# Kernel optimization log

Measured on AMD Instinct MI355X. Metric: run time of the kernel, lower is better.

## Reference

```python
import jax, jax.numpy as jnp
import numpy as np
import math

B, F, NB, H1, H2, K = 16384, 64, 64, 128, 128, 3
LN_EPS = 1e-5


def setup_inputs() -> dict:
    key = jax.random.key(0)
    ks = jax.random.split(key, 16)
    x = jax.random.normal(ks[0], (B, F), dtype=jnp.float32)
    # RBF params (per feature): centers init linspace(-3,3), log_widths = log(step)
    centers = jnp.broadcast_to(jnp.linspace(-3.0, 3.0, NB), (F, NB)).astype(jnp.float32)
    step = 6.0 / (NB - 1)
    log_widths = jnp.full((F, NB), math.log(step), dtype=jnp.float32)
    def lin(k, shape, fan_in):
        return jax.random.normal(k, shape, dtype=jnp.float32) / np.sqrt(fan_in)
    W1 = lin(ks[1], (F, NB, H1), NB); b1 = jnp.zeros((F, H1), jnp.float32)
    g1 = jnp.ones((F, H1), jnp.float32); be1 = jnp.zeros((F, H1), jnp.float32)
    W2 = lin(ks[2], (F, H1, H2), H1); b2 = jnp.zeros((F, H2), jnp.float32)
    g2 = jnp.ones((F, H2), jnp.float32); be2 = jnp.zeros((F, H2), jnp.float32)
    Wr = lin(ks[3], (F, NB, H2), NB); br = jnp.zeros((F, H2), jnp.float32)
    att = jnp.zeros((F,), jnp.float32)
    bias = jnp.zeros((H2,), jnp.float32)
    Wpi = lin(ks[4], (H2, K), H2); bpi = jnp.zeros((K,), jnp.float32)
    Wa = lin(ks[5], (H2, K), H2); ba = jnp.zeros((K,), jnp.float32)
    Wb = lin(ks[6], (H2, K), H2); bb = jnp.zeros((K,), jnp.float32)
    return dict(x=x, centers=centers, log_widths=log_widths, W1=W1, b1=b1, g1=g1,
                be1=be1, W2=W2, b2=b2, g2=g2, be2=be2, Wr=Wr, br=br, att=att,
                bias=bias, Wpi=Wpi, bpi=bpi, Wa=Wa, ba=ba, Wb=Wb, bb=bb)


def _layernorm(h, g, b):
    mu = jnp.mean(h, axis=-1, keepdims=True)
    var = jnp.mean((h - mu) ** 2, axis=-1, keepdims=True)
    return (h - mu) * jax.lax.rsqrt(var + LN_EPS) * g + b


def reference(x, centers, log_widths, W1, b1, g1, be1, W2, b2, g2, be2, Wr, br,
              att, bias, Wpi, bpi, Wa, ba, Wb, bb):
    # RBF expansion, feature axis batched: x [B,F] -> [B,F,NB]
    xc = jnp.clip(x, -10.0, 10.0)
    widths = jnp.exp(jnp.clip(log_widths, -5.0, 5.0)) + 0.1  # [F,NB]
    dist = (xc[:, :, None] - centers[None]) / widths[None]
    rbf = jnp.exp(-0.5 * jnp.clip(dist, -10.0, 10.0) ** 2)  # [B,F,NB]
    # per-feature MLP (grouped GEMMs via einsum)
    h = jnp.einsum('bfn,fnh->bfh', rbf, W1) + b1[None]
    h = jax.nn.gelu(_layernorm(h, g1[None], be1[None]), approximate=False)
    h = jnp.einsum('bfh,fhk->bfk', h, W2) + b2[None]
    h = jax.nn.gelu(_layernorm(h, g2[None], be2[None]), approximate=False)
    res = jnp.einsum('bfn,fnh->bfh', rbf, Wr) + br[None]
    stacked = h + 0.1 * res  # [B,F,H2]
    # attention-weighted aggregation over features
    w = jax.nn.softmax(att)
    agg = jnp.einsum('bfh,f->bh', stacked, w) + bias  # [B,H2]
    # mixture-beta head
    pi = jax.nn.softmax(agg @ Wpi + bpi, axis=-1)
    alpha = jnp.clip(jax.nn.softplus(agg @ Wa + ba) + 1.01, 1.01, 100.0)
    beta = jnp.clip(jax.nn.softplus(agg @ Wb + bb) + 1.01, 1.01, 100.0)
    pred = jnp.sum(pi * (alpha / (alpha + beta)), axis=-1)
    return jnp.clip(pred, 0.001, 0.999)
```

## Files before the change

### kernel.cpp

```cpp
#include <hip/hip_runtime.h>
#include <math.h>

#define BQ   16384
#define FQ   64
#define NBQ  64
#define HD   128
#define FG   4
#define FPG  16
#define MT   128
#define NT   512

typedef __attribute__((ext_vector_type(8))) short s16x8;
typedef __attribute__((ext_vector_type(4))) float f32x4;

__device__ __forceinline__ unsigned short f2bf(float x) {
    unsigned int u = __float_as_uint(x);
    return (unsigned short)((u + 0x7FFFu + ((u >> 16) & 1u)) >> 16);
}

__device__ __forceinline__ unsigned cvtpk_bf16(float lo, float hi) {
    unsigned r;
    asm("v_cvt_pk_bf16_f32 %0, %1, %2" : "=v"(r) : "v"(lo), "v"(hi));
    return r;
}

__device__ __forceinline__ float softplus_stable(float v) {
    return (v > 0.0f) ? (v + log1pf(expf(-v))) : log1pf(expf(v));
}

__device__ __forceinline__ f32x4 gelu4(f32x4 v) {
    const f32x4 v2 = v * v;
    const f32x4 tt = v2 * (-0.07135481f) + (-1.5957691f);
    const f32x4 s  = v * tt;
    f32x4 r;
    r[0] = __fdividef(v[0], 1.0f + __expf(s[0]));
    r[1] = __fdividef(v[1], 1.0f + __expf(s[1]));
    r[2] = __fdividef(v[2], 1.0f + __expf(s[2]));
    r[3] = __fdividef(v[3], 1.0f + __expf(s[3]));
    return r;
}

__device__ __forceinline__ void load16_lds(const unsigned short* g, unsigned short* l) {
    __builtin_amdgcn_global_load_lds(
        (const __attribute__((address_space(1))) unsigned int*)(uintptr_t)g,
        (__attribute__((address_space(3))) unsigned int*)(uintptr_t)l,
        16, 0, 0);
}


__global__ void __launch_bounds__(256) prep_misc(
    const float* __restrict__ att, const float* __restrict__ log_widths,
    const float* __restrict__ centers, const float* __restrict__ br,
    const float* __restrict__ bias,
    const float* __restrict__ b1, const float* __restrict__ g1, const float* __restrict__ be1,
    const float* __restrict__ b2, const float* __restrict__ g2, const float* __restrict__ be2,
    float* __restrict__ wsoft, float* __restrict__ crw2, float* __restrict__ rbias,
    float* __restrict__ Pk)
{
    const int t = threadIdx.x;
    if (blockIdx.x == 0) {
        __shared__ float ws[64];
        if (t < 64) {
            float v = att[t];
            float m = v;
#pragma unroll
            for (int s = 32; s >= 1; s >>= 1) m = fmaxf(m, __shfl_xor(m, s, 64));
            float e = expf(v - m);
            float ssum = e;
#pragma unroll
            for (int s = 32; s >= 1; s >>= 1) ssum += __shfl_xor(ssum, s, 64);
            const float w = e / ssum;
            ws[t] = w;
            wsoft[t] = w;
        }
        __syncthreads();
        for (int i = t; i < FQ * NBQ; i += 256) {
            float lw = fminf(fmaxf(log_widths[i], -5.0f), 5.0f);
            const float rw = 1.0f / (expf(lw) + 0.1f);
            ((float2*)crw2)[i] = make_float2(rw, -centers[i] * rw);
        }
        if (t < HD) {
            float s = bias[t];
            for (int f = 0; f < FQ; ++f) s += 0.1f * ws[f] * br[f * HD + t];
            rbias[t] = s;
        }
    } else {
        const int id = (blockIdx.x - 1) * 256 + t;
        if (id < FQ * 32) {
            float4* dst = (float4*)Pk + (size_t)id * 6;
            dst[0] = ((const float4*)b1)[id];
            dst[1] = ((const float4*)g1)[id];
            dst[2] = ((const float4*)be1)[id];
            dst[3] = ((const float4*)b2)[id];
            dst[4] = ((const float4*)g2)[id];
            dst[5] = ((const float4*)be2)[id];
        }
    }
}

__global__ void __launch_bounds__(256) prep_swz(
    const float* __restrict__ W1, const float* __restrict__ Wr, const float* __restrict__ W2,
    unsigned short* __restrict__ W1r, unsigned short* __restrict__ W2s)
{
    const int gid = blockIdx.x * 256 + threadIdx.x;
    const int l = gid & 63;
    const int r = l & 15;
    const int sig_base = ((r >> 2) << 3) + (r & 3);
    if (gid < 131072) {
        const int id = gid & 65535;
        const float* W    = (gid < 65536) ? W1 : Wr;
        const int half    = (gid < 65536) ? 0 : 8192;
        const int c  = (id >> 6) & 1;
        const int nt = (id >> 7) & 7;
        const int f  = id >> 10;
        const int hrow = ((nt >> 1) << 5) + ((nt & 1) << 2) + sig_base;
        const float* src = W + ((size_t)(f * 64 + c * 32 + (l >> 4) * 8)) * HD + hrow;
        s16x8 o;
#pragma unroll
        for (int j = 0; j < 8; ++j) o[j] = (short)f2bf(src[(size_t)j * HD]);
        *(s16x8*)(W1r + (size_t)f * 16384 + half + ((size_t)((nt * 2 + c) * 64 + l)) * 8) = o;
    } else {
        const int id = gid - 131072;
        const int c  = (id >> 6) & 3;
        const int nt = (id >> 8) & 7;
        const int f  = id >> 11;
        const int hrow = ((nt >> 1) << 5) + ((nt & 1) << 2) + sig_base;
        const float* src = W2 + ((size_t)(f * 128 + c * 32 + (l >> 4) * 8)) * HD + hrow;
        s16x8 o;
#pragma unroll
        for (int j = 0; j < 8; ++j) o[j] = (short)f2bf(src[(size_t)j * HD]);
        *(s16x8*)(W2s + (size_t)f * 16384 + ((size_t)((nt * 4 + c) * 64 + l)) * 8) = o;
    }
}

__global__ void __launch_bounds__(256) prep_xtr(const float* __restrict__ x,
                                                float* __restrict__ xT) {
    __shared__ float tile[64][65];
    const int t  = threadIdx.x;
    const int b0 = blockIdx.x * 64;
    {
        const int row = t & 63, cg = (t >> 6) * 16;
        const float4* src = (const float4*)(x + (size_t)(b0 + row) * FQ + cg);
#pragma unroll
        for (int i = 0; i < 4; ++i) {
            const float4 v = src[i];
            tile[row][cg + i * 4 + 0] = v.x;
            tile[row][cg + i * 4 + 1] = v.y;
            tile[row][cg + i * 4 + 2] = v.z;
            tile[row][cg + i * 4 + 3] = v.w;
        }
    }
    __syncthreads();
    {
        const int f = t >> 2, r0 = (t & 3) * 16;
        float* dst = xT + (size_t)f * BQ + b0 + r0;
#pragma unroll
        for (int i = 0; i < 16; ++i) dst[i] = tile[r0 + i][f];
    }
}

__global__ void __launch_bounds__(NT, 4) nam_main(
    const float* __restrict__ crw2,
    const float* __restrict__ xT,
    const unsigned short* __restrict__ W1r,
    const unsigned short* __restrict__ W2s,
    const float* __restrict__ Pk,
    const float* __restrict__ wsoft,
    float* __restrict__ agg)
{
    __shared__ __align__(16) unsigned short smem[32768];
    __shared__ __align__(16) float pkbuf[2][768];
    __shared__ __align__(16) float cwbuf[2][128];
    unsigned short* bufA = smem;
    unsigned short* bufB = smem + 16384;

    const int t  = threadIdx.x;
    const int ln = t & 63;
    const int wv = t >> 6;
    const int n  = ln & 15;
    const int q  = ln >> 4;
    const int fb = ln * 8;
    const int fg = blockIdx.x & 3;
    const int rb = blockIdx.x >> 2;
    const int b0 = rb * MT;

    f32x4 acc[8];
#pragma unroll
    for (int nt = 0; nt < 8; ++nt) acc[nt] = f32x4{0.f, 0.f, 0.f, 0.f};

    {
        const int f0 = fg * FPG + (rb & (FPG - 1));
        const unsigned short* g1r = W1r + (size_t)f0 * 16384;
        const unsigned short* gw2 = W2s + (size_t)f0 * 16384;
#pragma unroll
        for (int i = 0; i < 4; ++i) {
            const int chunk = i * 8 + wv;
            load16_lds(g1r + chunk * 512 + fb, bufA + chunk * 512);
        }
#pragma unroll
        for (int i = 0; i < 4; ++i) {
            const int chunk = i * 8 + wv;
            load16_lds(gw2 + chunk * 512 + fb, bufB + chunk * 512);
        }
        if (wv < 3)
            load16_lds((const unsigned short*)(Pk + (size_t)f0 * 768) + wv * 512 + ln * 8,
                       (unsigned short*)pkbuf[0] + wv * 512);
        if (wv == 3 && q < 2)
            load16_lds((const unsigned short*)(crw2 + (size_t)f0 * 128) + ln * 8,
                       (unsigned short*)cwbuf[0] + ln * 8);
    }

    for (int ff = 0; ff < FPG; ++ff) {
        const int f  = fg * FPG + ((ff + rb) & (FPG - 1));
        const int fn = fg * FPG + ((ff + 1 + rb) & (FPG - 1));
        const int p  = ff & 1;
        const float wf   = wsoft[f];
        const float wf01 = 0.1f * wf;

        float xv = xT[(size_t)f * BQ + b0 + wv * 16 + n];
        xv = fminf(fmaxf(xv, -10.0f), 10.0f);

        __syncthreads();

        s16x8 a0, a1;
        {
            const float4* c4 = (const float4*)cwbuf[p];
            unsigned pk[8];
#pragma unroll
            for (int h = 0; h < 2; ++h) {
#pragma unroll
                for (int i = 0; i < 4; ++i) {
                    const float4 cc = c4[h * 16 + q * 4 + i];
                    const float d0 = fmaf(xv, cc.x, cc.y);
                    const float d1 = fmaf(xv, cc.z, cc.w);
                    const float e0 = __expf(-0.5f * d0 * d0);
                    const float e1 = __expf(-0.5f * d1 * d1);
                    pk[h * 4 + i] = __builtin_amdgcn_perm(__float_as_uint(e1),
                                                          __float_as_uint(e0), 0x07060302u);
                }
            }
            int4 pa = make_int4(pk[0], pk[1], pk[2], pk[3]);
            int4 pb = make_int4(pk[4], pk[5], pk[6], pk[7]);
            a0 = *(s16x8*)&pa;
            a1 = *(s16x8*)&pb;
        }

        f32x4 hc[8];
#pragma unroll
        for (int nt = 0; nt < 8; ++nt) {
            const s16x8 w10 = *(const s16x8*)&bufA[(nt * 2 + 0) * 512 + fb];
            const s16x8 w11 = *(const s16x8*)&bufA[(nt * 2 + 1) * 512 + fb];
            f32x4 z = f32x4{0.f, 0.f, 0.f, 0.f};
            z = __builtin_amdgcn_mfma_f32_16x16x32_bf16(w10, a0, z, 0, 0, 0);
            z = __builtin_amdgcn_mfma_f32_16x16x32_bf16(w11, a1, z, 0, 0, 0);
            hc[nt] = z;
            const s16x8 wr0 = *(const s16x8*)&bufA[8192 + (nt * 2 + 0) * 512 + fb];
            const s16x8 wr1 = *(const s16x8*)&bufA[8192 + (nt * 2 + 1) * 512 + fb];
            f32x4 y = f32x4{0.f, 0.f, 0.f, 0.f};
            y = __builtin_amdgcn_mfma_f32_16x16x32_bf16(wr0, a0, y, 0, 0, 0);
            y = __builtin_amdgcn_mfma_f32_16x16x32_bf16(wr1, a1, y, 0, 0, 0);
            acc[nt] = y * wf01 + acc[nt];
        }

        const f32x4* pkf = (const f32x4*)pkbuf[p] + q * 12;
        f32x4 sm4 = {0.f, 0.f, 0.f, 0.f}, sq4 = {0.f, 0.f, 0.f, 0.f};
#pragma unroll
        for (int nt = 0; nt < 8; ++nt) {
            const f32x4 bg = pkf[(nt >> 1) * 48 + (nt & 1) * 6];
            const f32x4 v = hc[nt] + bg;
            hc[nt] = v; sm4 += v; sq4 += v * v;
        }
        float sm = (sm4[0] + sm4[1]) + (sm4[2] + sm4[3]);
        float sq = (sq4[0] + sq4[1]) + (sq4[2] + sq4[3]);
        sm += __shfl_xor(sm, 16); sm += __shfl_xor(sm, 32);
        sq += __shfl_xor(sq, 16); sq += __shfl_xor(sq, 32);
        const float mu = sm * (1.0f / 128.0f);
        const float rs = rsqrtf(sq * (1.0f / 128.0f) - mu * mu + 1e-5f);

        __syncthreads();

        if (ff < FPG - 1) {
            const unsigned short* g1r = W1r + (size_t)fn * 16384;
#pragma unroll
            for (int i = 0; i < 4; ++i) {
                const int chunk = i * 8 + wv;
                load16_lds(g1r + chunk * 512 + fb, bufA + chunk * 512);
            }
            if (wv < 3)
                load16_lds((const unsigned short*)(Pk + (size_t)fn * 768) + wv * 512 + ln * 8,
                           (unsigned short*)pkbuf[p ^ 1] + wv * 512);
            if (wv == 3 && q < 2)
                load16_lds((const unsigned short*)(crw2 + (size_t)fn * 128) + ln * 8,
                           (unsigned short*)cwbuf[p ^ 1] + ln * 8);
        }

        s16x8 bfr[4];
#pragma unroll
        for (int c = 0; c < 4; ++c) {
            const f32x4 gg0 = pkf[c * 48 + 1];
            const f32x4 bb0 = pkf[c * 48 + 2];
            const f32x4 gg1 = pkf[c * 48 + 6 + 1];
            const f32x4 bb1 = pkf[c * 48 + 6 + 2];
            const f32x4 z0 = gelu4((hc[2 * c]     - mu) * (gg0 * rs) + bb0);
            const f32x4 z1 = gelu4((hc[2 * c + 1] - mu) * (gg1 * rs) + bb1);
            int4 w = make_int4(cvtpk_bf16(z0[0], z0[1]), cvtpk_bf16(z0[2], z0[3]),
                               cvtpk_bf16(z1[0], z1[1]), cvtpk_bf16(z1[2], z1[3]));
            bfr[c] = *(s16x8*)&w;
        }

        f32x4 h2[8];
#pragma unroll
        for (int nt = 0; nt < 8; ++nt) {
            f32x4 z = f32x4{0.f, 0.f, 0.f, 0.f};
#pragma unroll
            for (int c = 0; c < 4; ++c) {
                const s16x8 w2f = *(const s16x8*)&bufB[(nt * 4 + c) * 512 + fb];
                z = __builtin_amdgcn_mfma_f32_16x16x32_bf16(w2f, bfr[c], z, 0, 0, 0);
            }
            h2[nt] = z;
        }

        __builtin_amdgcn_sched_barrier(0);
        __builtin_amdgcn_s_barrier();
        __builtin_amdgcn_sched_barrier(0);

        if (ff < FPG - 1) {
            const unsigned short* gw2 = W2s + (size_t)fn * 16384;
#pragma unroll
            for (int i = 0; i < 4; ++i) {
                const int chunk = i * 8 + wv;
                load16_lds(gw2 + chunk * 512 + fb, bufB + chunk * 512);
            }
        }

        f32x4 tm4 = {0.f, 0.f, 0.f, 0.f}, tq4 = {0.f, 0.f, 0.f, 0.f};
#pragma unroll
        for (int nt = 0; nt < 8; ++nt) {
            const f32x4 bg = pkf[(nt >> 1) * 48 + (nt & 1) * 6 + 3];
            const f32x4 v = h2[nt] + bg;
            h2[nt] = v; tm4 += v; tq4 += v * v;
        }
        float tm = (tm4[0] + tm4[1]) + (tm4[2] + tm4[3]);
        float tq = (tq4[0] + tq4[1]) + (tq4[2] + tq4[3]);
        tm += __shfl_xor(tm, 16); tm += __shfl_xor(tm, 32);
        tq += __shfl_xor(tq, 16); tq += __shfl_xor(tq, 32);
        const float mu2 = tm * (1.0f / 128.0f);
        const float rs2 = rsqrtf(tq * (1.0f / 128.0f) - mu2 * mu2 + 1e-5f);
#pragma unroll
        for (int nt = 0; nt < 8; ++nt) {
            const f32x4 gg = pkf[(nt >> 1) * 48 + (nt & 1) * 6 + 4];
            const f32x4 bb = pkf[(nt >> 1) * 48 + (nt & 1) * 6 + 5];
            const f32x4 y = (h2[nt] - mu2) * (gg * rs2) + bb;
            acc[nt] = gelu4(y) * wf + acc[nt];
        }
    }

    {
        float* fs = (float*)smem;
        const int r = wv * 16 + n;
#pragma unroll
        for (int nt = 0; nt < 8; ++nt) {
            const int col  = ((nt >> 1) << 5) + (q << 3) + ((nt & 1) << 2);
            const int byte = r * 512 + col * 4;
            const int sw   = byte ^ ((r & 7) << 4);
            *(f32x4*)((char*)fs + sw) = acc[nt];
        }
        __syncthreads();
        float* aggp = agg + (size_t)b0 * HD;
#pragma unroll
        for (int rr = 0; rr < 16; ++rr) {
            const int row = wv * 16 + rr;
#pragma unroll
            for (int half = 0; half < 2; ++half) {
                const int byte = row * 512 + half * 256 + ln * 4;
                const int sw   = byte ^ ((row & 7) << 4);
                const float v  = *(const float*)((const char*)fs + sw);
                atomicAdd(aggp + (size_t)row * HD + half * 64 + ln, v);
            }
        }
    }
}

__global__ void __launch_bounds__(256) nam_head(
    const float* __restrict__ agg, const float* __restrict__ rbias,
    const float* __restrict__ Wpi, const float* __restrict__ bpi,
    const float* __restrict__ Wa,  const float* __restrict__ ba,
    const float* __restrict__ Wb,  const float* __restrict__ bb,
    float* __restrict__ out)
{
    const int gid  = blockIdx.x * blockDim.x + threadIdx.x;
    const int row  = gid >> 6;
    const int lane = threadIdx.x & 63;
    if (row >= BQ) return;

    const float2 p  = ((const float2*)(agg + (size_t)row * HD))[lane];
    const float2 rb = ((const float2*)rbias)[lane];
    const float ax = p.x + rb.x;
    const float ay = p.y + rb.y;

    const float2* wp = (const float2*)Wpi;
    const float2* wa = (const float2*)Wa;
    const float2* wb = (const float2*)Wb;
    const float2 p01 = wp[lane * 3], p23 = wp[lane * 3 + 1], p45 = wp[lane * 3 + 2];
    const float2 a01 = wa[lane * 3], a23 = wa[lane * 3 + 1], a45 = wa[lane * 3 + 2];
    const float2 b01 = wb[lane * 3], b23 = wb[lane * 3 + 1], b45 = wb[lane * 3 + 2];

    float ppi0 = ax * p01.x + ay * p23.y;
    float ppi1 = ax * p01.y + ay * p45.x;
    float ppi2 = ax * p23.x + ay * p45.y;
    float pa0  = ax * a01.x + ay * a23.y;
    float pa1  = ax * a01.y + ay * a45.x;
    float pa2  = ax * a23.x + ay * a45.y;
    float pb0  = ax * b01.x + ay * b23.y;
    float pb1  = ax * b01.y + ay * b45.x;
    float pb2  = ax * b23.x + ay * b45.y;

#pragma unroll
    for (int s = 32; s >= 1; s >>= 1) {
        ppi0 += __shfl_xor(ppi0, s, 64);
        ppi1 += __shfl_xor(ppi1, s, 64);
        ppi2 += __shfl_xor(ppi2, s, 64);
        pa0  += __shfl_xor(pa0,  s, 64);
        pa1  += __shfl_xor(pa1,  s, 64);
        pa2  += __shfl_xor(pa2,  s, 64);
        pb0  += __shfl_xor(pb0,  s, 64);
        pb1  += __shfl_xor(pb1,  s, 64);
        pb2  += __shfl_xor(pb2,  s, 64);
    }

    if (lane == 0) {
        const float z0 = ppi0 + bpi[0], z1 = ppi1 + bpi[1], z2 = ppi2 + bpi[2];
        const float mz = fmaxf(z0, fmaxf(z1, z2));
        const float e0 = expf(z0 - mz), e1 = expf(z1 - mz), e2 = expf(z2 - mz);
        const float es = e0 + e1 + e2;

        const float al0 = fminf(fmaxf(softplus_stable(pa0 + ba[0]) + 1.01f, 1.01f), 100.0f);
        const float al1 = fminf(fmaxf(softplus_stable(pa1 + ba[1]) + 1.01f, 1.01f), 100.0f);
        const float al2 = fminf(fmaxf(softplus_stable(pa2 + ba[2]) + 1.01f, 1.01f), 100.0f);
        const float bt0 = fminf(fmaxf(softplus_stable(pb0 + bb[0]) + 1.01f, 1.01f), 100.0f);
        const float bt1 = fminf(fmaxf(softplus_stable(pb1 + bb[1]) + 1.01f, 1.01f), 100.0f);
        const float bt2 = fminf(fmaxf(softplus_stable(pb2 + bb[2]) + 1.01f, 1.01f), 100.0f);

        const float pred = (e0 * (al0 / (al0 + bt0))
                          + e1 * (al1 / (al1 + bt1))
                          + e2 * (al2 / (al2 + bt2))) / es;
        out[row] = fminf(fmaxf(pred, 0.001f), 0.999f);
    }
}

extern "C" void kernel_launch(void* const* d_in, const int* in_sizes, int n_in,
                              void* d_out, int out_size, void* d_ws, size_t ws_size,
                              hipStream_t stream) {
    const float* x          = (const float*)d_in[0];
    const float* centers    = (const float*)d_in[1];
    const float* log_widths = (const float*)d_in[2];
    const float* W1   = (const float*)d_in[3];
    const float* b1   = (const float*)d_in[4];
    const float* g1   = (const float*)d_in[5];
    const float* be1  = (const float*)d_in[6];
    const float* W2   = (const float*)d_in[7];
    const float* b2   = (const float*)d_in[8];
    const float* g2   = (const float*)d_in[9];
    const float* be2  = (const float*)d_in[10];
    const float* Wr   = (const float*)d_in[11];
    const float* br   = (const float*)d_in[12];
    const float* att  = (const float*)d_in[13];
    const float* bias = (const float*)d_in[14];
    const float* Wpi  = (const float*)d_in[15];
    const float* bpi  = (const float*)d_in[16];
    const float* Wa   = (const float*)d_in[17];
    const float* ba   = (const float*)d_in[18];
    const float* Wb   = (const float*)d_in[19];
    const float* bb   = (const float*)d_in[20];

    char* ws = (char*)d_ws;
    float*          wsoft = (float*)(ws + 0);
    float*          rbias = (float*)(ws + 1024);
    float*          crw2  = (float*)(ws + 8192);
    float*          Pk    = (float*)(ws + 65536);
    float*          xT    = (float*)(ws + 327680);
    unsigned short* W1r   = (unsigned short*)(ws + 4521984);
    unsigned short* W2s   = (unsigned short*)(ws + 6619136);
    float*          agg   = (float*)(ws + 8716288);

    prep_misc<<<9, 256, 0, stream>>>(att, log_widths, centers, br, bias,
                                     b1, g1, be1, b2, g2, be2,
                                     wsoft, crw2, rbias, Pk);
    prep_swz<<<1024, 256, 0, stream>>>(W1, Wr, W2, W1r, W2s);
    prep_xtr<<<256, 256, 0, stream>>>(x, xT);
    hipMemsetAsync(agg, 0, (size_t)BQ * HD * sizeof(float), stream);

    nam_main<<<(BQ / MT) * FG, NT, 0, stream>>>(crw2, xT, W1r, W2s, Pk,
                                                wsoft, agg);

    nam_head<<<BQ / 4, 256, 0, stream>>>(agg, rbias, Wpi, bpi, Wa, ba, Wb, bb,
                                         (float*)d_out);
}
```

Before: 390.1 us.

## Fuse prep kernels and memset into one launch, use exp2 and MFMA bias init

The three preprocessing kernels and the agg memset are merged into a single prep_all launch, with work partitioned by block index. This removes three launch and serialization gaps ahead of the main kernel. The RBF exponent and GELU are rewritten to use the native exp2 instruction, with the log2(e) factors folded into the precomputed width scale and the GELU constants. The LayerNorm pre-bias is now loaded as the MFMA accumulator's initial value, which removes a separate add pass. The result should match mathematically, though the folded constants change the rounding slightly.

```diff
diff --git a/kernel.cpp b/kernel.cpp
--- a/kernel.cpp
+++ b/kernel.cpp
@@ -30,13 +30,13 @@
 
 __device__ __forceinline__ f32x4 gelu4(f32x4 v) {
     const f32x4 v2 = v * v;
-    const f32x4 tt = v2 * (-0.07135481f) + (-1.5957691f);
+    const f32x4 tt = v2 * (-0.10294343f) + (-2.3022152f);
     const f32x4 s  = v * tt;
     f32x4 r;
-    r[0] = __fdividef(v[0], 1.0f + __expf(s[0]));
-    r[1] = __fdividef(v[1], 1.0f + __expf(s[1]));
-    r[2] = __fdividef(v[2], 1.0f + __expf(s[2]));
-    r[3] = __fdividef(v[3], 1.0f + __expf(s[3]));
+    r[0] = __fdividef(v[0], 1.0f + __builtin_amdgcn_exp2f(s[0]));
+    r[1] = __fdividef(v[1], 1.0f + __builtin_amdgcn_exp2f(s[1]));
+    r[2] = __fdividef(v[2], 1.0f + __builtin_amdgcn_exp2f(s[2]));
+    r[3] = __fdividef(v[3], 1.0f + __builtin_amdgcn_exp2f(s[3]));
     return r;
 }
 
@@ -48,18 +48,75 @@
 }
 
 
-__global__ void __launch_bounds__(256) prep_misc(
+__global__ void __launch_bounds__(256) prep_all(
     const float* __restrict__ att, const float* __restrict__ log_widths,
     const float* __restrict__ centers, const float* __restrict__ br,
     const float* __restrict__ bias,
     const float* __restrict__ b1, const float* __restrict__ g1, const float* __restrict__ be1,
     const float* __restrict__ b2, const float* __restrict__ g2, const float* __restrict__ be2,
+    const float* __restrict__ W1, const float* __restrict__ Wr, const float* __restrict__ W2,
+    const float* __restrict__ x,
     float* __restrict__ wsoft, float* __restrict__ crw2, float* __restrict__ rbias,
-    float* __restrict__ Pk)
+    float* __restrict__ Pk, unsigned short* __restrict__ W1r,
+    unsigned short* __restrict__ W2s, float* __restrict__ xT, float* __restrict__ agg)
 {
-    const int t = threadIdx.x;
-    if (blockIdx.x == 0) {
-        __shared__ float ws[64];
+    const int bid = blockIdx.x;
+    const int t   = threadIdx.x;
+    __shared__ float tile[64][65];
+
+    if (bid < 1024) {
+        const int gid = bid * 256 + t;
+        const int l = gid & 63;
+        const int r = l & 15;
+        const int sig_base = ((r >> 2) << 3) + (r & 3);
+        if (gid < 131072) {
+            const int id = gid & 65535;
+            const float* W = (gid < 65536) ? W1 : Wr;
+            const int half = (gid < 65536) ? 0 : 8192;
+            const int c  = (id >> 6) & 1;
+            const int nt = (id >> 7) & 7;
+            const int f  = id >> 10;
+            const int hrow = ((nt >> 1) << 5) + ((nt & 1) << 2) + sig_base;
+            const float* src = W + ((size_t)(f * 64 + c * 32 + (l >> 4) * 8)) * HD + hrow;
+            s16x8 o;
+#pragma unroll
+            for (int j = 0; j < 8; ++j) o[j] = (short)f2bf(src[(size_t)j * HD]);
+            *(s16x8*)(W1r + (size_t)f * 16384 + half + ((size_t)((nt * 2 + c) * 64 + l)) * 8) = o;
+        } else {
+            const int id = gid - 131072;
+            const int c  = (id >> 6) & 3;
+            const int nt = (id >> 8) & 7;
+            const int f  = id >> 11;
+            const int hrow = ((nt >> 1) << 5) + ((nt & 1) << 2) + sig_base;
+            const float* src = W2 + ((size_t)(f * 128 + c * 32 + (l >> 4) * 8)) * HD + hrow;
+            s16x8 o;
+#pragma unroll
+            for (int j = 0; j < 8; ++j) o[j] = (short)f2bf(src[(size_t)j * HD]);
+            *(s16x8*)(W2s + (size_t)f * 16384 + ((size_t)((nt * 4 + c) * 64 + l)) * 8) = o;
+        }
+    } else if (bid < 1280) {
+        const int b0 = (bid - 1024) * 64;
+        {
+            const int row = t & 63, cg = (t >> 6) * 16;
+            const float4* src = (const float4*)(x + (size_t)(b0 + row) * FQ + cg);
+#pragma unroll
+            for (int i = 0; i < 4; ++i) {
+                const float4 v = src[i];
+                tile[row][cg + i * 4 + 0] = v.x;
+                tile[row][cg + i * 4 + 1] = v.y;
+                tile[row][cg + i * 4 + 2] = v.z;
+                tile[row][cg + i * 4 + 3] = v.w;
+            }
+        }
+        __syncthreads();
+        {
+            const int f = t >> 2, r0 = (t & 3) * 16;
+            float* dst = xT + (size_t)f * BQ + b0 + r0;
+#pragma unroll
+            for (int i = 0; i < 16; ++i) dst[i] = tile[r0 + i][f];
+        }
+    } else if (bid == 1280) {
+        float* ws = &tile[0][0];
         if (t < 64) {
             float v = att[t];
             float m = v;
@@ -76,86 +133,29 @@
         __syncthreads();
         for (int i = t; i < FQ * NBQ; i += 256) {
             float lw = fminf(fmaxf(log_widths[i], -5.0f), 5.0f);
-            const float rw = 1.0f / (expf(lw) + 0.1f);
-            ((float2*)crw2)[i] = make_float2(rw, -centers[i] * rw);
+            const float rwq = 0.84932179f / (expf(lw) + 0.1f);
+            ((float2*)crw2)[i] = make_float2(rwq, -centers[i] * rwq);
         }
         if (t < HD) {
             float s = bias[t];
             for (int f = 0; f < FQ; ++f) s += 0.1f * ws[f] * br[f * HD + t];
             rbias[t] = s;
         }
+    } else if (bid < 1289) {
+        const int id = (bid - 1281) * 256 + t;
+        float4* dst = (float4*)Pk + (size_t)id * 6;
+        dst[0] = ((const float4*)b1)[id];
+        dst[1] = ((const float4*)g1)[id];
+        dst[2] = ((const float4*)be1)[id];
+        dst[3] = ((const float4*)b2)[id];
+        dst[4] = ((const float4*)g2)[id];
+        dst[5] = ((const float4*)be2)[id];
     } else {
-        const int id = (blockIdx.x - 1) * 256 + t;
-        if (id < FQ * 32) {
-            float4* dst = (float4*)Pk + (size_t)id * 6;
-            dst[0] = ((const float4*)b1)[id];
-            dst[1] = ((const float4*)g1)[id];
-            dst[2] = ((const float4*)be1)[id];
-            dst[3] = ((const float4*)b2)[id];
-            dst[4] = ((const float4*)g2)[id];
-            dst[5] = ((const float4*)be2)[id];
-        }
-    }
-}
-
-__global__ void __launch_bounds__(256) prep_swz(
-    const float* __restrict__ W1, const float* __restrict__ Wr, const float* __restrict__ W2,
-    unsigned short* __restrict__ W1r, unsigned short* __restrict__ W2s)
-{
-    const int gid = blockIdx.x * 256 + threadIdx.x;
-    const int l = gid & 63;
-    const int r = l & 15;
-    const int sig_base = ((r >> 2) << 3) + (r & 3);
-    if (gid < 131072) {
-        const int id = gid & 65535;
-        const float* W    = (gid < 65536) ? W1 : Wr;
-        const int half    = (gid < 65536) ? 0 : 8192;
-        const int c  = (id >> 6) & 1;
-        const int nt = (id >> 7) & 7;
-        const int f  = id >> 10;
-        const int hrow = ((nt >> 1) << 5) + ((nt & 1) << 2) + sig_base;
-        const float* src = W + ((size_t)(f * 64 + c * 32 + (l >> 4) * 8)) * HD + hrow;
-        s16x8 o;
-#pragma unroll
-        for (int j = 0; j < 8; ++j) o[j] = (short)f2bf(src[(size_t)j * HD]);
-        *(s16x8*)(W1r + (size_t)f * 16384 + half + ((size_t)((nt * 2 + c) * 64 + l)) * 8) = o;
-    } else {
-        const int id = gid - 131072;
-        const int c  = (id >> 6) & 3;
-        const int nt = (id >> 8) & 7;
-        const int f  = id >> 11;
-        const int hrow = ((nt >> 1) << 5) + ((nt & 1) << 2) + sig_base;
-        const float* src = W2 + ((size_t)(f * 128 + c * 32 + (l >> 4) * 8)) * HD + hrow;
-        s16x8 o;
-#pragma unroll
-        for (int j = 0; j < 8; ++j) o[j] = (short)f2bf(src[(size_t)j * HD]);
-        *(s16x8*)(W2s + (size_t)f * 16384 + ((size_t)((nt * 4 + c) * 64 + l)) * 8) = o;
-    }
-}
-
-__global__ void __launch_bounds__(256) prep_xtr(const float* __restrict__ x,
-                                                float* __restrict__ xT) {
-    __shared__ float tile[64][65];
-    const int t  = threadIdx.x;
-    const int b0 = blockIdx.x * 64;
-    {
-        const int row = t & 63, cg = (t >> 6) * 16;
-        const float4* src = (const float4*)(x + (size_t)(b0 + row) * FQ + cg);
-#pragma unroll
-        for (int i = 0; i < 4; ++i) {
-            const float4 v = src[i];
-            tile[row][cg + i * 4 + 0] = v.x;
-            tile[row][cg + i * 4 + 1] = v.y;
-            tile[row][cg + i * 4 + 2] = v.z;
-            tile[row][cg + i * 4 + 3] = v.w;
-        }
-    }
-    __syncthreads();
-    {
-        const int f = t >> 2, r0 = (t & 3) * 16;
-        float* dst = xT + (size_t)f * BQ + b0 + r0;
-#pragma unroll
-        for (int i = 0; i < 16; ++i) dst[i] = tile[r0 + i][f];
+        const int zb = bid - 1289;
+        float4* dst = (float4*)agg + (size_t)zb * 8192 + t;
+        const float4 z = make_float4(0.f, 0.f, 0.f, 0.f);
+#pragma unroll
+        for (int i = 0; i < 32; ++i) dst[i * 256] = z;
     }
 }
 
@@ -233,8 +233,8 @@
                     const float4 cc = c4[h * 16 + q * 4 + i];
                     const float d0 = fmaf(xv, cc.x, cc.y);
                     const float d1 = fmaf(xv, cc.z, cc.w);
-                    const float e0 = __expf(-0.5f * d0 * d0);
-                    const float e1 = __expf(-0.5f * d1 * d1);
+                    const float e0 = __builtin_amdgcn_exp2f(-(d0 * d0));
+                    const float e1 = __builtin_amdgcn_exp2f(-(d1 * d1));
                     pk[h * 4 + i] = __builtin_amdgcn_perm(__float_as_uint(e1),
                                                           __float_as_uint(e0), 0x07060302u);
                 }
@@ -245,12 +245,14 @@
             a1 = *(s16x8*)&pb;
         }
 
+        const f32x4* pkf = (const f32x4*)pkbuf[p] + q * 12;
+
         f32x4 hc[8];
 #pragma unroll
         for (int nt = 0; nt < 8; ++nt) {
             const s16x8 w10 = *(const s16x8*)&bufA[(nt * 2 + 0) * 512 + fb];
             const s16x8 w11 = *(const s16x8*)&bufA[(nt * 2 + 1) * 512 + fb];
-            f32x4 z = f32x4{0.f, 0.f, 0.f, 0.f};
+            f32x4 z = pkf[(nt >> 1) * 48 + (nt & 1) * 6];
             z = __builtin_amdgcn_mfma_f32_16x16x32_bf16(w10, a0, z, 0, 0, 0);
             z = __builtin_amdgcn_mfma_f32_16x16x32_bf16(w11, a1, z, 0, 0, 0);
             hc[nt] = z;
@@ -262,13 +264,11 @@
             acc[nt] = y * wf01 + acc[nt];
         }
 
-        const f32x4* pkf = (const f32x4*)pkbuf[p] + q * 12;
         f32x4 sm4 = {0.f, 0.f, 0.f, 0.f}, sq4 = {0.f, 0.f, 0.f, 0.f};
 #pragma unroll
         for (int nt = 0; nt < 8; ++nt) {
-            const f32x4 bg = pkf[(nt >> 1) * 48 + (nt & 1) * 6];
-            const f32x4 v = hc[nt] + bg;
-            hc[nt] = v; sm4 += v; sq4 += v * v;
+            const f32x4 v = hc[nt];
+            sm4 += v; sq4 += v * v;
         }
         float sm = (sm4[0] + sm4[1]) + (sm4[2] + sm4[3]);
         float sq = (sq4[0] + sq4[1]) + (sq4[2] + sq4[3]);
@@ -311,7 +311,7 @@
         f32x4 h2[8];
 #pragma unroll
         for (int nt = 0; nt < 8; ++nt) {
-            f32x4 z = f32x4{0.f, 0.f, 0.f, 0.f};
+            f32x4 z = pkf[(nt >> 1) * 48 + (nt & 1) * 6 + 3];
 #pragma unroll
             for (int c = 0; c < 4; ++c) {
                 const s16x8 w2f = *(const s16x8*)&bufB[(nt * 4 + c) * 512 + fb];
@@ -336,9 +336,8 @@
         f32x4 tm4 = {0.f, 0.f, 0.f, 0.f}, tq4 = {0.f, 0.f, 0.f, 0.f};
 #pragma unroll
         for (int nt = 0; nt < 8; ++nt) {
-            const f32x4 bg = pkf[(nt >> 1) * 48 + (nt & 1) * 6 + 3];
-            const f32x4 v = h2[nt] + bg;
-            h2[nt] = v; tm4 += v; tq4 += v * v;
+            const f32x4 v = h2[nt];
+            tm4 += v; tq4 += v * v;
         }
         float tm = (tm4[0] + tm4[1]) + (tm4[2] + tm4[3]);
         float tq = (tq4[0] + tq4[1]) + (tq4[2] + tq4[3]);
@@ -483,12 +482,10 @@
     unsigned short* W2s   = (unsigned short*)(ws + 6619136);
     float*          agg   = (float*)(ws + 8716288);
 
-    prep_misc<<<9, 256, 0, stream>>>(att, log_widths, centers, br, bias,
-                                     b1, g1, be1, b2, g2, be2,
-                                     wsoft, crw2, rbias, Pk);
-    prep_swz<<<1024, 256, 0, stream>>>(W1, Wr, W2, W1r, W2s);
-    prep_xtr<<<256, 256, 0, stream>>>(x, xT);
-    hipMemsetAsync(agg, 0, (size_t)BQ * HD * sizeof(float), stream);
+    prep_all<<<1353, 256, 0, stream>>>(att, log_widths, centers, br, bias,
+                                       b1, g1, be1, b2, g2, be2,
+                                       W1, Wr, W2, x,
+                                       wsoft, crw2, rbias, Pk, W1r, W2s, xT, agg);
 
     nam_main<<<(BQ / MT) * FG, NT, 0, stream>>>(crw2, xT, W1r, W2s, Pk,
                                                 wsoft, agg);
```

Result: faster. 374.6 us (median of 2 runs) (-4.0%).
